# Kernel tuning notes

Hardware: AMD Instinct MI355X
Metric: run time of the kernel (lower is better)

## Reference

```python
import jax, jax.numpy as jnp
import numpy as np

V, E, H, K, B, T = 50000, 300, 256, 25, 64, 256


def setup_inputs() -> dict:
    key = jax.random.key(0)
    ks = jax.random.split(key, 20)
    g = lambda k, shape, s=0.05: (jax.random.normal(k, shape, dtype=jnp.float32) * s)
    return {
        "sentence": jax.random.randint(ks[0], (B, T), 0, V),
        "labels": jax.random.randint(ks[1], (B, T), 0, K),
        "mask": jnp.ones((B, T), dtype=bool),
        "emb_table": g(ks[2], (V, E), 0.1),
        "w_ih_f": g(ks[3], (4 * H, E)),
        "w_hh_f": g(ks[4], (4 * H, H)),
        "b_ih_f": g(ks[5], (4 * H,)),
        "b_hh_f": g(ks[6], (4 * H,)),
        "w_ih_b": g(ks[7], (4 * H, E)),
        "w_hh_b": g(ks[8], (4 * H, H)),
        "b_ih_b": g(ks[9], (4 * H,)),
        "b_hh_b": g(ks[10], (4 * H,)),
        "W_out": g(ks[11], (K, 2 * H)),
        "b_out": g(ks[12], (K,)),
        "start_trans": g(ks[13], (K,), 0.1),
        "end_trans": g(ks[14], (K,), 0.1),
        "trans": g(ks[15], (K, K), 0.1),
    }


def _lstm_dir(x, w_ih, w_hh, b_ih, b_hh, reverse):
    # x: [T, B, E] -> hs: [T, B, H]; torch gate order i,f,g,o
    xg = jnp.einsum('tbe,ge->tbg', x, w_ih) + b_ih + b_hh  # [T,B,4H]
    h0 = jnp.zeros((x.shape[1], w_hh.shape[1]), x.dtype)

    def step(carry, g_t):
        h, c = carry
        gates = g_t + h @ w_hh.T
        i, f, gg, o = jnp.split(gates, 4, axis=-1)
        c = jax.nn.sigmoid(f) * c + jax.nn.sigmoid(i) * jnp.tanh(gg)
        h = jax.nn.sigmoid(o) * jnp.tanh(c)
        return (h, c), h

    _, hs = jax.lax.scan(step, (h0, h0), xg, reverse=reverse)
    return hs


def _crf_nll(emissions, labels, mask, start_trans, end_trans, trans):
    # emissions: [B,T,K]; returns sum over batch of -(log-likelihood)
    maskf = mask.astype(emissions.dtype)
    # --- numerator: score of the gold path ---
    em_sc = jnp.take_along_axis(emissions, labels[..., None], axis=-1)[..., 0]  # [B,T]
    tr_sc = trans[labels[:, :-1], labels[:, 1:]]  # [B,T-1]
    seq_ends = jnp.sum(mask.astype(jnp.int32), axis=1) - 1  # [B]
    last_tags = jnp.take_along_axis(labels, seq_ends[:, None], axis=1)[:, 0]
    num = (start_trans[labels[:, 0]] + em_sc[:, 0]
           + jnp.sum((em_sc[:, 1:] + tr_sc) * maskf[:, 1:], axis=1)
           + end_trans[last_tags])  # [B]
    # --- denominator: forward algorithm (sequential logsumexp scan) ---
    alpha0 = start_trans + emissions[:, 0]  # [B,K]
    em_rest = emissions[:, 1:].transpose(1, 0, 2)  # [T-1,B,K]
    m_rest = maskf[:, 1:].T  # [T-1,B]

    def step(alpha, xs):
        e_t, m_t = xs
        nxt = jax.nn.logsumexp(alpha[:, :, None] + trans[None] + e_t[:, None, :], axis=1)
        alpha = jnp.where(m_t[:, None] > 0, nxt, alpha)
        return alpha, None

    alpha, _ = jax.lax.scan(step, alpha0, (em_rest, m_rest))
    logZ = jax.nn.logsumexp(alpha + end_trans, axis=-1)  # [B]
    return jnp.sum(logZ - num)


def reference(sentence, labels, mask, emb_table,
              w_ih_f, w_hh_f, b_ih_f, b_hh_f,
              w_ih_b, w_hh_b, b_ih_b, b_hh_b,
              W_out, b_out, start_trans, end_trans, trans):
    x = emb_table[sentence].transpose(1, 0, 2)  # [T,B,E]
    hf = _lstm_dir(x, w_ih_f, w_hh_f, b_ih_f, b_hh_f, reverse=False)
    hb = _lstm_dir(x, w_ih_b, w_hh_b, b_ih_b, b_hh_b, reverse=True)
    h = jnp.concatenate([hf, hb], axis=-1)  # [T,B,2H]  (dropout = identity, eval)
    emissions = (h @ W_out.T + b_out).transpose(1, 0, 2)  # [B,T,K]
    return _crf_nll(emissions, labels, mask, start_trans, end_trans, trans)
```

## Files before the change

### kernel.cpp

```cpp
#include <hip/hip_runtime.h>
#include <math.h>

#define B_ 64
#define T_ 256
#define E_ 300
#define EP 160
#define H_ 256
#define K_ 25
#define G4 1024
#define M_ (B_*T_)

#define QL 18
#define QS 14

typedef _Float16 h2v __attribute__((ext_vector_type(2)));
typedef _Float16 f16x8 __attribute__((ext_vector_type(8)));
typedef float f32x4 __attribute__((ext_vector_type(4)));

__device__ __forceinline__ float sigm(float x) {
    return __builtin_amdgcn_rcpf(1.0f + __expf(-x));
}
__device__ __forceinline__ float tanhfast(float x) {
    return 1.0f - 2.0f * __builtin_amdgcn_rcpf(1.0f + __expf(2.0f * x));
}
__device__ __forceinline__ h2v asH2(unsigned u) { return __builtin_bit_cast(h2v, u); }
__device__ __forceinline__ unsigned pack_h2(float a, float b) {
    union { _Float16 h[2]; unsigned u; } cv;
    cv.h[0] = (_Float16)a; cv.h[1] = (_Float16)b; return cv.u;
}

__global__ __launch_bounds__(256) void prep_kernel(
    const float* __restrict__ w_ih_f, const float* __restrict__ b_ih_f,
    const float* __restrict__ b_hh_f, const float* __restrict__ w_ih_b,
    const float* __restrict__ b_ih_b, const float* __restrict__ b_hh_b,
    unsigned* __restrict__ wP, float* __restrict__ biasC)
{
    int idx = blockIdx.x * 256 + threadIdx.x;
    if (idx < 2*EP*G4) {
        int d = idx / (EP*G4); int rem = idx % (EP*G4);
        int kp = rem / G4, n = rem % G4;
        int u = n >> 2, g = n & 3;
        const float* w = d ? w_ih_b : w_ih_f;
        float a = 0.f, bb = 0.f;
        if (kp < 150) { a = w[(g*H_+u)*E_ + 2*kp]; bb = w[(g*H_+u)*E_ + 2*kp + 1]; }
        wP[idx] = pack_h2(a, bb);
    }
    if (idx < 2*G4) {
        int d = idx >> 10; int n = idx & 1023;
        int u = n >> 2, g = n & 3;
        biasC[idx] = d ? (b_ih_b[g*H_+u] + b_hh_b[g*H_+u])
                       : (b_ih_f[g*H_+u] + b_hh_f[g*H_+u]);
    }
}

__global__ __launch_bounds__(256) void scale_kernel(
    const float* __restrict__ w_hh_f, const float* __restrict__ w_hh_b,
    float* __restrict__ swF)
{
    int row = blockIdx.x*4 + (threadIdx.x >> 6);
    int lane = threadIdx.x & 63;
    int d = row >> 10, rr = row & 1023;
    const float* w = (d ? w_hh_b : w_hh_f) + (size_t)rr*H_;
    float m = 0.f;
    #pragma unroll
    for (int q = 0; q < 4; q++) m = fmaxf(m, fabsf(w[lane + q*64]));
    #pragma unroll
    for (int off = 32; off; off >>= 1) m = fmaxf(m, __shfl_down(m, off));
    if (lane == 0) {
        int g = rr >> 8, j = rr & 255;
        swF[(d*H_ + j)*4 + g] = fmaxf(m, 1e-20f) / 127.f;
    }
}

__global__ __launch_bounds__(256) void quant_kernel(
    const float* __restrict__ w_hh_f, const float* __restrict__ w_hh_b,
    const float* __restrict__ swF, uint4* __restrict__ wqL, uint4* __restrict__ wqS)
{
    int idx = blockIdx.x*256 + threadIdx.x;
    if (idx >= 2*64*256) return;
    int d = idx >> 14, q = (idx >> 8) & 63, j = idx & 255;
    const float* w = d ? w_hh_b : w_hh_f;
    unsigned words[4];
    #pragma unroll
    for (int g = 0; g < 4; g++) {
        float s = swF[(d*H_ + j)*4 + g];
        unsigned wd = 0;
        #pragma unroll
        for (int kk = 0; kk < 4; kk++) {
            float v = w[(size_t)(g*H_ + j)*H_ + 4*q + kk] / s;
            int q8 = (int)__builtin_rintf(v);
            q8 = q8 > 127 ? 127 : (q8 < -127 ? -127 : q8);
            wd |= ((unsigned)(q8 & 0xFF)) << (8*kk);
        }
        words[g] = wd;
    }
    uint4 W = make_uint4(words[0], words[1], words[2], words[3]);
    int kh = q >> 5, qq = q & 31;
    if (qq < QL) wqL[((size_t)d*2*QL + kh*QL + qq)*256 + j] = W;
    else         wqS[((size_t)d*2*QS + kh*QS + (qq-QL))*256 + j] = W;
}

__global__ __launch_bounds__(256) void gather_kernel(const int* __restrict__ sent,
    const float* __restrict__ emb, unsigned* __restrict__ xP)
{
    int idx = blockIdx.x * 256 + threadIdx.x;
    if (idx >= EP*M_) return;
    int kp = idx >> 14;
    int tb = idx & (M_-1);
    float a = 0.f, b = 0.f;
    if (kp < 150) {
        const float* er = emb + (size_t)sent[tb]*E_;
        a = er[2*kp]; b = er[2*kp+1];
    }
    xP[idx] = pack_h2(a, b);
}

__global__ __launch_bounds__(256) void gemm_xg_kernel(const unsigned* __restrict__ xP,
    const unsigned* __restrict__ wP, const float* __restrict__ biasC, unsigned* __restrict__ xgu)
{
    __shared__ unsigned As[16][132];
    __shared__ unsigned Bs[16][132];
    __shared__ unsigned Cs[128][66];
    int bx = blockIdx.x & 15;
    int by = blockIdx.x >> 4;
    int row0 = by*128, col0 = bx*128;
    int d = col0 >> 10, g0 = col0 & 1023;
    const unsigned* wPd = wP + (size_t)d*(EP*G4);
    int tid = threadIdx.x;
    int lane = tid & 63, wid = tid >> 6;
    int wm = wid >> 1, wn = wid & 1;
    int lg = lane >> 4, lr = lane & 15;
    int kpL = tid >> 4, colL = (tid & 15) * 8;
    f32x4 acc[4][4];
    #pragma unroll
    for (int i = 0; i < 4; i++)
        #pragma unroll
        for (int jj = 0; jj < 4; jj++) acc[i][jj] = (f32x4){0.f,0.f,0.f,0.f};

    for (int kk = 0; kk < EP; kk += 16) {
        const unsigned* ga = &xP [(size_t)(kk + kpL)*M_ + row0 + colL];
        const unsigned* gb = &wPd[(size_t)(kk + kpL)*G4 + g0  + colL];
        *(uint4*)&As[kpL][colL]   = *(const uint4*)ga;
        *(uint4*)&As[kpL][colL+4] = *(const uint4*)(ga+4);
        *(uint4*)&Bs[kpL][colL]   = *(const uint4*)gb;
        *(uint4*)&Bs[kpL][colL+4] = *(const uint4*)(gb+4);
        __syncthreads();
        union U { unsigned u[4]; f16x8 v; };
        U af[4], bf[4];
        #pragma unroll
        for (int f = 0; f < 4; f++)
            #pragma unroll
            for (int e2 = 0; e2 < 4; e2++) {
                af[f].u[e2] = As[lg*4 + e2][wm*64 + f*16 + lr];
                bf[f].u[e2] = Bs[lg*4 + e2][wn*64 + f*16 + lr];
            }
        #pragma unroll
        for (int fm = 0; fm < 4; fm++)
            #pragma unroll
            for (int fn = 0; fn < 4; fn++)
                acc[fm][fn] = __builtin_amdgcn_mfma_f32_16x16x32_f16(
                    bf[fn].v, af[fm].v, acc[fm][fn], 0, 0, 0);
        __syncthreads();
    }
    #pragma unroll
    for (int fn = 0; fn < 4; fn++) {
        int n4 = wn*64 + fn*16 + lg*4;
        float b0 = biasC[d*G4 + g0 + n4],     b1 = biasC[d*G4 + g0 + n4 + 1];
        float b2 = biasC[d*G4 + g0 + n4 + 2], b3 = biasC[d*G4 + g0 + n4 + 3];
        #pragma unroll
        for (int fm = 0; fm < 4; fm++) {
            int row = wm*64 + fm*16 + lr;
            Cs[row][(n4>>1)]     = pack_h2(acc[fm][fn][0] + b0, acc[fm][fn][1] + b1);
            Cs[row][(n4>>1) + 1] = pack_h2(acc[fm][fn][2] + b2, acc[fm][fn][3] + b3);
        }
    }
    __syncthreads();
    for (int i = tid; i < 128*64; i += 256) {
        int r = i >> 6, cc = i & 63;
        xgu[((size_t)d*M_ + row0 + r)*512 + (g0 >> 1) + cc] = Cs[r][cc];
    }
}

__global__ __launch_bounds__(512, 2) void lstm_kernel(
    const uint4* __restrict__ wqL, const uint4* __restrict__ wqS,
    const float4* __restrict__ swF4, const unsigned* __restrict__ xgu,
    float* __restrict__ hs)
{
    int blk = blockIdx.x;
    int d = blk >> 6, b = blk & 63;
    int tid = threadIdx.x;
    int kh = tid >> 8, j = tid & 255;

    __shared__ uint4 wlds[2*QL][256];
    __shared__ int4 part[256];
    __shared__ __align__(16) unsigned hq[64];

    for (int i = tid; i < 2*QS*256; i += 512)
        wlds[i >> 8][i & 255] = wqS[(size_t)d*2*QS*256 + i];
    __syncthreads();
    uint4 rv[QS];
    #pragma unroll
    for (int s = 0; s < QS; s++) rv[s] = wlds[kh*QS + s][j];
    __syncthreads();
    for (int i = tid; i < 2*QL*256; i += 512)
        wlds[i >> 8][i & 255] = wqL[(size_t)d*2*QL*256 + i];
    if (tid < 64) hq[tid] = 0u;

    const unsigned* xgp = xgu + ((size_t)d*M_ + (size_t)b*T_)*512;
    float* hsp = hs + ((size_t)(d*B_ + b)*T_)*H_;
    int t0 = d ? T_-1 : 0;
    int dt = d ? -1 : 1;
    float4 sc = make_float4(0.f,0.f,0.f,0.f);
    uint2 xw = make_uint2(0u, 0u);
    if (!kh) {
        float4 s0 = ((const float4*)swF4)[d*H_ + j];
        sc = make_float4(s0.x*(1.f/127.f), s0.y*(1.f/127.f),
                         s0.z*(1.f/127.f), s0.w*(1.f/127.f));
        xw = *(const uint2*)&xgp[t0*512 + 2*j];
    }
    float c = 0.f;
    __syncthreads();

    int t = t0;
    #pragma unroll 1
    for (int tt = 0; tt < T_; tt++) {
        int a0 = 0, a1 = 0, a2 = 0, a3 = 0;
        const uint4* hb = ((const uint4*)hq) + kh*8;
        #pragma unroll
        for (int qg = 0; qg < 8; qg++) {
            uint4 hw4 = hb[qg];
            #pragma unroll
            for (int e = 0; e < 4; e++) {
                int ql = qg*4 + e;
                unsigned hw = (e==0)?hw4.x:(e==1)?hw4.y:(e==2)?hw4.z:hw4.w;
                uint4 w4 = (ql < QL) ? wlds[kh*QL + ql][j] : rv[ql - QL];
                a0 = __builtin_amdgcn_sdot4((int)w4.x, (int)hw, a0, false);
                a1 = __builtin_amdgcn_sdot4((int)w4.y, (int)hw, a1, false);
                a2 = __builtin_amdgcn_sdot4((int)w4.z, (int)hw, a2, false);
                a3 = __builtin_amdgcn_sdot4((int)w4.w, (int)hw, a3, false);
            }
        }
        if (kh) part[j] = make_int4(a0, a1, a2, a3);
        __syncthreads();
        if (!kh) {
            int4 p1 = part[j];
            h2v x01 = asH2(xw.x), x23 = asH2(xw.y);
            float gi = (float)(a0 + p1.x)*sc.x + (float)x01[0];
            float gf = (float)(a1 + p1.y)*sc.y + (float)x01[1];
            float gg = (float)(a2 + p1.z)*sc.z + (float)x23[0];
            float go = (float)(a3 + p1.w)*sc.w + (float)x23[1];
            c = sigm(gf)*c + sigm(gi)*tanhfast(gg);
            float h = sigm(go)*tanhfast(c);
            hsp[(size_t)t*H_ + j] = h;
            int q8 = (int)__builtin_rintf(h * 127.f);
            ((char*)hq)[j] = (char)q8;
            if (tt < T_-1) xw = *(const uint2*)&xgp[(t+dt)*512 + 2*j];
        }
        t += dt;
        __syncthreads();
    }
}

__global__ __launch_bounds__(256) void emis_kernel(const float* __restrict__ hs,
    const float* __restrict__ W_out, const float* __restrict__ b_out, float* __restrict__ em)
{
    int idx = blockIdx.x*256 + threadIdx.x;
    if (idx >= M_*K_) return;
    int tb = idx / K_, k = idx % K_;
    const float4* hf = (const float4*)(hs + (size_t)tb*H_);
    const float4* hb = (const float4*)(hs + (size_t)B_*T_*H_ + (size_t)tb*H_);
    const float4* w0 = (const float4*)(W_out + (size_t)k*2*H_);
    const float4* w1 = w0 + H_/4;
    float s = b_out[k];
    #pragma unroll 8
    for (int q = 0; q < H_/4; q++) {
        float4 h = hf[q], w = w0[q];
        s += h.x*w.x + h.y*w.y + h.z*w.z + h.w*w.w;
    }
    #pragma unroll 8
    for (int q = 0; q < H_/4; q++) {
        float4 h = hb[q], w = w1[q];
        s += h.x*w.x + h.y*w.y + h.z*w.z + h.w*w.w;
    }
    em[idx] = s;
}

__global__ void zero_kernel(float* out) { out[0] = 0.f; }

__global__ __launch_bounds__(64) void crf_kernel(const float* __restrict__ em,
    const int* __restrict__ labels, const float* __restrict__ start_t,
    const float* __restrict__ end_t, const float* __restrict__ trans,
    float* __restrict__ out)
{
    int b = blockIdx.x, lane = threadIdx.x;
    const int* lab = labels + b*T_;
    const float* emr = em + (size_t)b*T_*K_;

    float part = 0.f;
    for (int t = lane; t < T_; t += 64) {
        int lt = lab[t];
        part += emr[t*K_ + lt];
        part += (t == 0) ? start_t[lt] : trans[lab[t-1]*K_ + lt];
    }
    if (lane == 0) part += end_t[lab[T_-1]];
    #pragma unroll
    for (int off = 32; off; off >>= 1) part += __shfl_down(part, off);

    bool act = lane < K_;
    float trc[K_];
    #pragma unroll
    for (int i = 0; i < K_; i++) trc[i] = act ? trans[i*K_ + lane] : 0.f;
    float alpha = act ? (start_t[lane] + emr[lane]) : -1e30f;
    float ej = act ? emr[K_ + lane] : 0.f;
    #pragma unroll 1
    for (int t = 1; t < T_; t++) {
        float ej_next = (t+1 < T_ && act) ? emr[(t+1)*K_ + lane] : 0.f;
        float vals[K_];
        float m = -1e30f;
        #pragma unroll
        for (int i = 0; i < K_; i++) {
            float ai = __shfl(alpha, i);
            vals[i] = ai + trc[i];
            m = fmaxf(m, vals[i]);
        }
        float s = 0.f;
        #pragma unroll
        for (int i = 0; i < K_; i++) s += __expf(vals[i] - m);
        float na = __logf(s) + m + ej;
        alpha = act ? na : -1e30f;
        ej = ej_next;
    }
    float v = act ? (alpha + end_t[lane]) : -1e30f;
    float m = v;
    #pragma unroll
    for (int off = 32; off; off >>= 1) m = fmaxf(m, __shfl_down(m, off));
    m = __shfl(m, 0);
    float s = act ? __expf(v - m) : 0.f;
    #pragma unroll
    for (int off = 32; off; off >>= 1) s += __shfl_down(s, off);
    if (lane == 0) {
        float logZ = __logf(s) + m;
        atomicAdd(out, logZ - part);
    }
}

extern "C" void kernel_launch(void* const* d_in, const int* in_sizes, int n_in,
                              void* d_out, int out_size, void* d_ws, size_t ws_size,
                              hipStream_t stream)
{
    const int*   sentence = (const int*)  d_in[0];
    const int*   labels   = (const int*)  d_in[1];
    const float* emb      = (const float*)d_in[3];
    const float* w_ih_f   = (const float*)d_in[4];
    const float* w_hh_f   = (const float*)d_in[5];
    const float* b_ih_f   = (const float*)d_in[6];
    const float* b_hh_f   = (const float*)d_in[7];
    const float* w_ih_b   = (const float*)d_in[8];
    const float* w_hh_b   = (const float*)d_in[9];
    const float* b_ih_b   = (const float*)d_in[10];
    const float* b_hh_b   = (const float*)d_in[11];
    const float* W_out    = (const float*)d_in[12];
    const float* b_out    = (const float*)d_in[13];
    const float* start_t  = (const float*)d_in[14];
    const float* end_t    = (const float*)d_in[15];
    const float* trans    = (const float*)d_in[16];

    char* ws = (char*)d_ws;
    unsigned* xP  = (unsigned*)(ws);
    unsigned* xgu = (unsigned*)(ws + 10485760);
    unsigned* wP  = (unsigned*)(ws + 77594624);
    float*    swF = (float*)   (ws + 78905344);
    uint4*    wqL = (uint4*)   (ws + 78913536);
    uint4*    wqS = (uint4*)   (ws + 79208448);
    float*  biasC = (float*)   (ws + 79437824);
    float*    hs  = (float*)   (ws + 79446016);
    float*    em  = (float*)   (ws + 113000448);

    prep_kernel<<<1280, 256, 0, stream>>>(w_ih_f, b_ih_f, b_hh_f,
                                          w_ih_b, b_ih_b, b_hh_b, wP, biasC);
    scale_kernel<<<512, 256, 0, stream>>>(w_hh_f, w_hh_b, swF);
    quant_kernel<<<128, 256, 0, stream>>>(w_hh_f, w_hh_b, swF, wqL, wqS);
    gather_kernel<<<(EP*M_)/256, 256, 0, stream>>>(sentence, emb, xP);
    gemm_xg_kernel<<<128*16, 256, 0, stream>>>(xP, wP, biasC, xgu);
    lstm_kernel<<<128, 512, 0, stream>>>(wqL, wqS, (const float4*)swF, xgu, hs);
    emis_kernel<<<(M_*K_ + 255)/256, 256, 0, stream>>>(hs, W_out, b_out, em);
    zero_kernel<<<1, 1, 0, stream>>>((float*)d_out);
    crf_kernel<<<B_, 64, 0, stream>>>(em, labels, start_t, end_t, trans, (float*)d_out);
}
```

Before: 573.1 us.

## Pack LDS-resident recurrent weights as int4 and stage embedding gather through LDS

The first 72 columns of each half of the recurrent weight matrix, the part held in LDS, are now quantized to 4-bit with a separate per-row scale. Each byte holds two nibbles, which the kernel unpacks by shift and mask before feeding two sdot4 ops. This halves the LDS footprint and the LDS read traffic per step on the latency-bound recurrence, at the cost of extra ALU work and lower weight precision. The embedding gather now builds a tile in shared memory and writes the transposed layout with coalesced stores.

```diff
diff --git a/kernel.cpp b/kernel.cpp
--- a/kernel.cpp
+++ b/kernel.cpp
@@ -10,7 +10,7 @@
 #define G4 1024
 #define M_ (B_*T_)
 
-#define QL 18
+#define P4 9
 #define QS 14
 
 typedef _Float16 h2v __attribute__((ext_vector_type(2)));
@@ -27,6 +27,9 @@
 __device__ __forceinline__ unsigned pack_h2(float a, float b) {
     union { _Float16 h[2]; unsigned u; } cv;
     cv.h[0] = (_Float16)a; cv.h[1] = (_Float16)b; return cv.u;
+}
+__device__ __forceinline__ int clampi(int v, int lo, int hi) {
+    return v < lo ? lo : (v > hi ? hi : v);
 }
 
 __global__ __launch_bounds__(256) void prep_kernel(
@@ -55,64 +58,108 @@
 
 __global__ __launch_bounds__(256) void scale_kernel(
     const float* __restrict__ w_hh_f, const float* __restrict__ w_hh_b,
-    float* __restrict__ swF)
+    float* __restrict__ swF4, float* __restrict__ swF8)
 {
     int row = blockIdx.x*4 + (threadIdx.x >> 6);
     int lane = threadIdx.x & 63;
     int d = row >> 10, rr = row & 1023;
     const float* w = (d ? w_hh_b : w_hh_f) + (size_t)rr*H_;
-    float m = 0.f;
-    #pragma unroll
-    for (int q = 0; q < 4; q++) m = fmaxf(m, fabsf(w[lane + q*64]));
-    #pragma unroll
-    for (int off = 32; off; off >>= 1) m = fmaxf(m, __shfl_down(m, off));
+    float m4 = 0.f, m8 = 0.f;
+    #pragma unroll
+    for (int q = 0; q < 4; q++) {
+        int k = lane + q*64;
+        float v = fabsf(w[k]);
+        if ((k & 127) < 72) m4 = fmaxf(m4, v); else m8 = fmaxf(m8, v);
+    }
+    #pragma unroll
+    for (int off = 32; off; off >>= 1) {
+        m4 = fmaxf(m4, __shfl_down(m4, off));
+        m8 = fmaxf(m8, __shfl_down(m8, off));
+    }
     if (lane == 0) {
         int g = rr >> 8, j = rr & 255;
-        swF[(d*H_ + j)*4 + g] = fmaxf(m, 1e-20f) / 127.f;
+        swF4[(d*H_ + j)*4 + g] = fmaxf(m4, 1e-20f) / 7.f;
+        swF8[(d*H_ + j)*4 + g] = fmaxf(m8, 1e-20f) / 127.f;
     }
 }
 
 __global__ __launch_bounds__(256) void quant_kernel(
     const float* __restrict__ w_hh_f, const float* __restrict__ w_hh_b,
-    const float* __restrict__ swF, uint4* __restrict__ wqL, uint4* __restrict__ wqS)
+    const float* __restrict__ swF4, const float* __restrict__ swF8,
+    uint4* __restrict__ wq4, uint4* __restrict__ wqS)
 {
     int idx = blockIdx.x*256 + threadIdx.x;
-    if (idx >= 2*64*256) return;
-    int d = idx >> 14, q = (idx >> 8) & 63, j = idx & 255;
-    const float* w = d ? w_hh_b : w_hh_f;
-    unsigned words[4];
-    #pragma unroll
-    for (int g = 0; g < 4; g++) {
-        float s = swF[(d*H_ + j)*4 + g];
-        unsigned wd = 0;
-        #pragma unroll
-        for (int kk = 0; kk < 4; kk++) {
-            float v = w[(size_t)(g*H_ + j)*H_ + 4*q + kk] / s;
-            int q8 = (int)__builtin_rintf(v);
-            q8 = q8 > 127 ? 127 : (q8 < -127 ? -127 : q8);
-            wd |= ((unsigned)(q8 & 0xFF)) << (8*kk);
-        }
-        words[g] = wd;
-    }
-    uint4 W = make_uint4(words[0], words[1], words[2], words[3]);
-    int kh = q >> 5, qq = q & 31;
-    if (qq < QL) wqL[((size_t)d*2*QL + kh*QL + qq)*256 + j] = W;
-    else         wqS[((size_t)d*2*QS + kh*QS + (qq-QL))*256 + j] = W;
+    if (idx < 2*2*P4*256) {
+        int d  = idx / (2*P4*256);
+        int kh = (idx / (P4*256)) % 2;
+        int p  = (idx / 256) % P4;
+        int j  = idx & 255;
+        const float* w = d ? w_hh_b : w_hh_f;
+        unsigned words[4];
+        #pragma unroll
+        for (int g = 0; g < 4; g++) {
+            float s4 = swF4[(d*H_ + j)*4 + g];
+            float inv = 1.0f / s4;
+            unsigned wd = 0;
+            #pragma unroll
+            for (int kk = 0; kk < 4; kk++) {
+                int k0 = kh*128 + 8*p + kk;
+                int qh = clampi((int)__builtin_rintf(w[(size_t)(g*H_+j)*H_ + k0]*inv), -7, 7);
+                int ql = clampi((int)__builtin_rintf(w[(size_t)(g*H_+j)*H_ + k0+4]*inv), -7, 7);
+                unsigned byte = (((unsigned)qh & 0xFu) << 4) | ((unsigned)ql & 0xFu);
+                wd |= byte << (8*kk);
+            }
+            words[g] = wd;
+        }
+        wq4[idx] = make_uint4(words[0], words[1], words[2], words[3]);
+    }
+    if (idx < 2*2*QS*256) {
+        int d  = idx / (2*QS*256);
+        int kh = (idx / (QS*256)) % 2;
+        int s  = (idx / 256) % QS;
+        int j  = idx & 255;
+        const float* w = d ? w_hh_b : w_hh_f;
+        unsigned words[4];
+        #pragma unroll
+        for (int g = 0; g < 4; g++) {
+            float s8 = swF8[(d*H_ + j)*4 + g];
+            float inv = 1.0f / s8;
+            unsigned wd = 0;
+            #pragma unroll
+            for (int kk = 0; kk < 4; kk++) {
+                int k = kh*128 + 4*(18+s) + kk;
+                int q8 = clampi((int)__builtin_rintf(w[(size_t)(g*H_+j)*H_ + k]*inv), -127, 127);
+                wd |= ((unsigned)(q8 & 0xFF)) << (8*kk);
+            }
+            words[g] = wd;
+        }
+        wqS[idx] = make_uint4(words[0], words[1], words[2], words[3]);
+    }
 }
 
 __global__ __launch_bounds__(256) void gather_kernel(const int* __restrict__ sent,
     const float* __restrict__ emb, unsigned* __restrict__ xP)
 {
-    int idx = blockIdx.x * 256 + threadIdx.x;
-    if (idx >= EP*M_) return;
-    int kp = idx >> 14;
-    int tb = idx & (M_-1);
-    float a = 0.f, b = 0.f;
-    if (kp < 150) {
-        const float* er = emb + (size_t)sent[tb]*E_;
-        a = er[2*kp]; b = er[2*kp+1];
-    }
-    xP[idx] = pack_h2(a, b);
+    __shared__ unsigned xl[64][153];
+    int tb0 = blockIdx.x * 64;
+    int tid = threadIdx.x;
+    #pragma unroll 1
+    for (int i = tid; i < 64*152; i += 256) {
+        int r  = i / 152;
+        int kp = i - r*152;
+        unsigned v = 0;
+        if (kp < 150) {
+            const float* er = emb + (size_t)sent[tb0 + r]*E_;
+            v = pack_h2(er[2*kp], er[2*kp+1]);
+        }
+        if (kp < 152) xl[r][kp] = v;
+    }
+    __syncthreads();
+    #pragma unroll 1
+    for (int i = tid; i < 160*64; i += 256) {
+        int kp = i >> 6, l = i & 63;
+        xP[(size_t)kp*M_ + tb0 + l] = (kp < 150) ? xl[l][kp] : 0u;
+    }
 }
 
 __global__ __launch_bounds__(256) void gemm_xg_kernel(const unsigned* __restrict__ xP,
@@ -182,40 +229,54 @@
 }
 
 __global__ __launch_bounds__(512, 2) void lstm_kernel(
-    const uint4* __restrict__ wqL, const uint4* __restrict__ wqS,
-    const float4* __restrict__ swF4, const unsigned* __restrict__ xgu,
-    float* __restrict__ hs)
+    const uint4* __restrict__ wq4, const uint4* __restrict__ wqS,
+    const float4* __restrict__ swF4v, const float4* __restrict__ swF8v,
+    const unsigned* __restrict__ xgu, float* __restrict__ hs)
 {
     int blk = blockIdx.x;
     int d = blk >> 6, b = blk & 63;
     int tid = threadIdx.x;
     int kh = tid >> 8, j = tid & 255;
 
-    __shared__ uint4 wlds[2*QL][256];
-    __shared__ int4 part[256];
+    __shared__ uint4 wlds4[2][P4][256];
+    __shared__ int4 part4[256];
+    __shared__ int4 part8[256];
     __shared__ __align__(16) unsigned hq[64];
 
-    for (int i = tid; i < 2*QS*256; i += 512)
-        wlds[i >> 8][i & 255] = wqS[(size_t)d*2*QS*256 + i];
-    __syncthreads();
+    uint4* wflat = &wlds4[0][0][0];
+
     uint4 rv[QS];
-    #pragma unroll
-    for (int s = 0; s < QS; s++) rv[s] = wlds[kh*QS + s][j];
-    __syncthreads();
-    for (int i = tid; i < 2*QL*256; i += 512)
-        wlds[i >> 8][i & 255] = wqL[(size_t)d*2*QL*256 + i];
+    #pragma unroll 1
+    for (int pass = 0; pass < 2; pass++) {
+        int base = pass * 18;
+        int nrows = (2*QS - base) < 18 ? (2*QS - base) : 18;
+        for (int i = tid; i < nrows*256; i += 512)
+            wflat[i] = wqS[(size_t)d*2*QS*256 + ((size_t)base << 8) + i];
+        __syncthreads();
+        #pragma unroll
+        for (int s = 0; s < QS; s++) {
+            int r = kh*QS + s;
+            if (r >= base && r < base + nrows) rv[s] = wflat[(r - base)*256 + j];
+        }
+        __syncthreads();
+    }
+    for (int i = tid; i < 2*P4*256; i += 512)
+        wflat[i] = wq4[(size_t)d*2*P4*256 + i];
     if (tid < 64) hq[tid] = 0u;
 
     const unsigned* xgp = xgu + ((size_t)d*M_ + (size_t)b*T_)*512;
     float* hsp = hs + ((size_t)(d*B_ + b)*T_)*H_;
     int t0 = d ? T_-1 : 0;
     int dt = d ? -1 : 1;
-    float4 sc = make_float4(0.f,0.f,0.f,0.f);
+    float4 sc4 = make_float4(0.f,0.f,0.f,0.f);
+    float4 sc8 = make_float4(0.f,0.f,0.f,0.f);
     uint2 xw = make_uint2(0u, 0u);
     if (!kh) {
-        float4 s0 = ((const float4*)swF4)[d*H_ + j];
-        sc = make_float4(s0.x*(1.f/127.f), s0.y*(1.f/127.f),
-                         s0.z*(1.f/127.f), s0.w*(1.f/127.f));
+        float4 s4 = ((const float4*)swF4v)[d*H_ + j];
+        float4 s8 = ((const float4*)swF8v)[d*H_ + j];
+        const float f4 = 1.f/(16.f*127.f), f8 = 1.f/127.f;
+        sc4 = make_float4(s4.x*f4, s4.y*f4, s4.z*f4, s4.w*f4);
+        sc8 = make_float4(s8.x*f8, s8.y*f8, s8.z*f8, s8.w*f8);
         xw = *(const uint2*)&xgp[t0*512 + 2*j];
     }
     float c = 0.f;
@@ -224,31 +285,56 @@
     int t = t0;
     #pragma unroll 1
     for (int tt = 0; tt < T_; tt++) {
-        int a0 = 0, a1 = 0, a2 = 0, a3 = 0;
-        const uint4* hb = ((const uint4*)hq) + kh*8;
-        #pragma unroll
-        for (int qg = 0; qg < 8; qg++) {
-            uint4 hw4 = hb[qg];
-            #pragma unroll
-            for (int e = 0; e < 4; e++) {
-                int ql = qg*4 + e;
-                unsigned hw = (e==0)?hw4.x:(e==1)?hw4.y:(e==2)?hw4.z:hw4.w;
-                uint4 w4 = (ql < QL) ? wlds[kh*QL + ql][j] : rv[ql - QL];
-                a0 = __builtin_amdgcn_sdot4((int)w4.x, (int)hw, a0, false);
-                a1 = __builtin_amdgcn_sdot4((int)w4.y, (int)hw, a1, false);
-                a2 = __builtin_amdgcn_sdot4((int)w4.z, (int)hw, a2, false);
-                a3 = __builtin_amdgcn_sdot4((int)w4.w, (int)hw, a3, false);
-            }
-        }
-        if (kh) part[j] = make_int4(a0, a1, a2, a3);
+        uint4 hb[8];
+        const uint4* hbase = ((const uint4*)hq) + kh*8;
+        #pragma unroll
+        for (int q = 0; q < 8; q++) hb[q] = hbase[q];
+        int a40 = 0, a41 = 0, a42 = 0, a43 = 0;
+        int a80 = 0, a81 = 0, a82 = 0, a83 = 0;
+        #pragma unroll
+        for (int p = 0; p < P4; p++) {
+            uint4 w4 = wlds4[kh][p][j];
+            int wh = 2*p, wl = 2*p + 1;
+            uint4 vh = hb[wh>>2], vl = hb[wl>>2];
+            unsigned hh = ((wh&3)==0)?vh.x:((wh&3)==1)?vh.y:((wh&3)==2)?vh.z:vh.w;
+            unsigned hl = ((wl&3)==0)?vl.x:((wl&3)==1)?vl.y:((wl&3)==2)?vl.z:vl.w;
+            unsigned hi, lo;
+            hi = w4.x & 0xF0F0F0F0u; lo = (w4.x << 4) & 0xF0F0F0F0u;
+            a40 = __builtin_amdgcn_sdot4((int)hi, (int)hh, a40, false);
+            a40 = __builtin_amdgcn_sdot4((int)lo, (int)hl, a40, false);
+            hi = w4.y & 0xF0F0F0F0u; lo = (w4.y << 4) & 0xF0F0F0F0u;
+            a41 = __builtin_amdgcn_sdot4((int)hi, (int)hh, a41, false);
+            a41 = __builtin_amdgcn_sdot4((int)lo, (int)hl, a41, false);
+            hi = w4.z & 0xF0F0F0F0u; lo = (w4.z << 4) & 0xF0F0F0F0u;
+            a42 = __builtin_amdgcn_sdot4((int)hi, (int)hh, a42, false);
+            a42 = __builtin_amdgcn_sdot4((int)lo, (int)hl, a42, false);
+            hi = w4.w & 0xF0F0F0F0u; lo = (w4.w << 4) & 0xF0F0F0F0u;
+            a43 = __builtin_amdgcn_sdot4((int)hi, (int)hh, a43, false);
+            a43 = __builtin_amdgcn_sdot4((int)lo, (int)hl, a43, false);
+        }
+        #pragma unroll
+        for (int s = 0; s < QS; s++) {
+            uint4 w4 = rv[s];
+            int wi = 18 + s;
+            uint4 vv = hb[wi>>2];
+            unsigned hw = ((wi&3)==0)?vv.x:((wi&3)==1)?vv.y:((wi&3)==2)?vv.z:vv.w;
+            a80 = __builtin_amdgcn_sdot4((int)w4.x, (int)hw, a80, false);
+            a81 = __builtin_amdgcn_sdot4((int)w4.y, (int)hw, a81, false);
+            a82 = __builtin_amdgcn_sdot4((int)w4.z, (int)hw, a82, false);
+            a83 = __builtin_amdgcn_sdot4((int)w4.w, (int)hw, a83, false);
+        }
+        if (kh) {
+            part4[j] = make_int4(a40, a41, a42, a43);
+            part8[j] = make_int4(a80, a81, a82, a83);
+        }
         __syncthreads();
         if (!kh) {
-            int4 p1 = part[j];
+            int4 p4 = part4[j], p8 = part8[j];
             h2v x01 = asH2(xw.x), x23 = asH2(xw.y);
-            float gi = (float)(a0 + p1.x)*sc.x + (float)x01[0];
-            float gf = (float)(a1 + p1.y)*sc.y + (float)x01[1];
-            float gg = (float)(a2 + p1.z)*sc.z + (float)x23[0];
-            float go = (float)(a3 + p1.w)*sc.w + (float)x23[1];
+            float gi = (float)(a40 + p4.x)*sc4.x + (float)(a80 + p8.x)*sc8.x + (float)x01[0];
+            float gf = (float)(a41 + p4.y)*sc4.y + (float)(a81 + p8.y)*sc8.y + (float)x01[1];
+            float gg = (float)(a42 + p4.z)*sc4.z + (float)(a82 + p8.z)*sc8.z + (float)x23[0];
+            float go = (float)(a43 + p4.w)*sc4.w + (float)(a83 + p8.w)*sc8.w + (float)x23[1];
             c = sigm(gf)*c + sigm(gi)*tanhfast(gg);
             float h = sigm(go)*tanhfast(c);
             hsp[(size_t)t*H_ + j] = h;
@@ -366,23 +452,25 @@
     const float* trans    = (const float*)d_in[16];
 
     char* ws = (char*)d_ws;
-    unsigned* xP  = (unsigned*)(ws);
-    unsigned* xgu = (unsigned*)(ws + 10485760);
-    unsigned* wP  = (unsigned*)(ws + 77594624);
-    float*    swF = (float*)   (ws + 78905344);
-    uint4*    wqL = (uint4*)   (ws + 78913536);
-    uint4*    wqS = (uint4*)   (ws + 79208448);
-    float*  biasC = (float*)   (ws + 79437824);
-    float*    hs  = (float*)   (ws + 79446016);
-    float*    em  = (float*)   (ws + 113000448);
+    unsigned* xP   = (unsigned*)(ws);
+    unsigned* xgu  = (unsigned*)(ws + 10485760);
+    unsigned* wP   = (unsigned*)(ws + 77594624);
+    float*    swF4 = (float*)   (ws + 78905344);
+    float*    swF8 = (float*)   (ws + 78913536);
+    uint4*    wq4  = (uint4*)   (ws + 78921728);
+    uint4*    wqS  = (uint4*)   (ws + 79069184);
+    float*  biasC  = (float*)   (ws + 79527936);
+    float*    hs   = (float*)   (ws + 79536128);
+    float*    em   = (float*)   (ws + 113090560);
 
     prep_kernel<<<1280, 256, 0, stream>>>(w_ih_f, b_ih_f, b_hh_f,
                                           w_ih_b, b_ih_b, b_hh_b, wP, biasC);
-    scale_kernel<<<512, 256, 0, stream>>>(w_hh_f, w_hh_b, swF);
-    quant_kernel<<<128, 256, 0, stream>>>(w_hh_f, w_hh_b, swF, wqL, wqS);
-    gather_kernel<<<(EP*M_)/256, 256, 0, stream>>>(sentence, emb, xP);
+    scale_kernel<<<512, 256, 0, stream>>>(w_hh_f, w_hh_b, swF4, swF8);
+    quant_kernel<<<112, 256, 0, stream>>>(w_hh_f, w_hh_b, swF4, swF8, wq4, wqS);
+    gather_kernel<<<M_/64, 256, 0, stream>>>(sentence, emb, xP);
     gemm_xg_kernel<<<128*16, 256, 0, stream>>>(xP, wP, biasC, xgu);
-    lstm_kernel<<<128, 512, 0, stream>>>(wqL, wqS, (const float4*)swF, xgu, hs);
+    lstm_kernel<<<128, 512, 0, stream>>>(wq4, wqS, (const float4*)swF4,
+                                         (const float4*)swF8, xgu, hs);
     emis_kernel<<<(M_*K_ + 255)/256, 256, 0, stream>>>(hs, W_out, b_out, em);
     zero_kernel<<<1, 1, 0, stream>>>((float*)d_out);
     crf_kernel<<<B_, 64, 0, stream>>>(em, labels, start_t, end_t, trans, (float*)d_out);
```

New measurement: 685.2 us. +19.6%, slower.
